# Kernel optimization log

Hardware: AMD Instinct MI355X
Metric: run time of the kernel (lower is better)

## Reference

```python
import jax, jax.numpy as jnp
import numpy as np

HID = 512
VOCAB = 64
SAMPLE_PROB = 0.1


def lstm_cell(x, h, c, w_ih, w_hh, b_ih, b_hh):
    # PyTorch LSTMCell: gates ordered (i, f, g, o)
    gates = x @ w_ih.T + b_ih + h @ w_hh.T + b_hh
    i, f, g, o = jnp.split(gates, 4, axis=-1)
    i = jax.nn.sigmoid(i)
    f = jax.nn.sigmoid(f)
    g = jnp.tanh(g)
    o = jax.nn.sigmoid(o)
    c_new = f * c + i * g
    h_new = o * jnp.tanh(c_new)
    return h_new, c_new


def _linear_params(key, out_dim, in_dim):
    bound = 1.0 / np.sqrt(in_dim)
    kw, kb = jax.random.split(key)
    w = jax.random.uniform(kw, (out_dim, in_dim), jnp.float32, -bound, bound)
    b = jax.random.uniform(kb, (out_dim,), jnp.float32, -bound, bound)
    return w, b


def setup_inputs() -> dict:
    key = jax.random.key(0)
    ks = jax.random.split(key, 9)
    B, R, T = 128, 512, 128
    phi_w, phi_b = _linear_params(ks[0], HID, HID)          # decoder -> context
    psi_w, psi_b = _linear_params(ks[1], HID, HID)          # listener -> context
    w_ih0, b_ih0 = _linear_params(ks[2], 4 * HID, HID + VOCAB)
    w_hh0, b_hh0 = _linear_params(ks[3], 4 * HID, HID)
    w_ih1, b_ih1 = _linear_params(ks[4], 4 * HID, HID)
    w_hh1, b_hh1 = _linear_params(ks[5], 4 * HID, HID)
    out_w, out_b = _linear_params(ks[6], VOCAB, HID)
    h = jax.random.normal(ks[7], (B, R, HID), jnp.float32)
    y = jax.random.randint(ks[8], (B, T + 1), 0, VOCAB)
    return dict(h=h, phi_w=phi_w, phi_b=phi_b, psi_w=psi_w, psi_b=psi_b,
                w_ih0=w_ih0, w_hh0=w_hh0, b_ih0=b_ih0, b_hh0=b_hh0,
                w_ih1=w_ih1, w_hh1=w_hh1, b_ih1=b_ih1, b_hh1=b_hh1,
                out_w=out_w, out_b=out_b, y=y)


def reference(h, phi_w, phi_b, psi_w, psi_b,
              w_ih0, w_hh0, b_ih0, b_hh0,
              w_ih1, w_hh1, b_ih1, b_hh1,
              out_w, out_b, y):
    B = h.shape[0]
    T = y.shape[1] - 1
    # psi is applied to h identically every step; hoist it out of the loop.
    hp = h @ psi_w.T + psi_b                     # [B, R, HID]
    keys = jax.random.split(jax.random.key(42), T)
    z0 = y[:, 0]
    zeros = jnp.zeros((B, HID), h.dtype)
    carry0 = (zeros, zeros, zeros, zeros, z0)    # s0, cs0, s1, cs1, z

    def step(carry, xs):
        s0, cs0, s1, cs1, z = carry
        key, y_next = xs
        z_oh = jax.nn.one_hot(z, VOCAB, dtype=h.dtype)
        # additive-style attention context
        sq = s1 @ phi_w.T + phi_b                # [B, HID]
        e = jnp.einsum('bd,brd->br', sq, hp)     # [B, R]
        alpha = jax.nn.softmax(e, axis=1)
        c = jnp.einsum('br,brd->bd', alpha, hp)  # [B, HID]
        inp = jnp.concatenate([z_oh, c], axis=1)
        s0, cs0 = lstm_cell(inp, s0, cs0, w_ih0, w_hh0, b_ih0, b_hh0)
        s1, cs1 = lstm_cell(s0, s1, cs1, w_ih1, w_hh1, b_ih1, b_hh1)
        o = s1 @ out_w.T + out_b                 # [B, VOCAB]
        k1, k2 = jax.random.split(key)
        sampled = jax.random.categorical(k1, o, axis=1)
        do_sample = jax.random.bernoulli(k2, SAMPLE_PROB, (B,))
        z_next = jnp.where(do_sample, sampled, y_next)
        return (s0, cs0, s1, cs1, z_next), o

    xs = (keys, y[:, 1:].T)                      # per-step key, teacher token [T, B]
    _, outs = jax.lax.scan(step, carry0, xs)     # outs: [T, B, VOCAB]
    return jnp.transpose(outs, (1, 0, 2))        # [B, T, VOCAB]
```

## Files before the change

### kernel.cpp

```cpp
#include <hip/hip_runtime.h>
#include <math.h>


#define JAX_PARTITIONABLE 1

#define B_   128
#define HID_ 512
#define VOC_ 64
#define T_   128

#define S0_OFF    0u
#define CS0_OFF   65536u
#define S1_OFF    131072u
#define CS1_OFF   196608u
#define SQT_OFF   262144u
#define CPR_OFF   327680u
#define AMAT_OFF  393216u
#define W1PSI_OFF 655360u
#define BIAS0_OFF 1703936u
#define V_OFF     1705984u
#define PART_OFF  1706496u
#define GUM_OFF   5900800u
#define UB_OFF    6949376u
#define Z_OFF     6965760u

#define TF_TINY 1.17549435e-38f

__device__ __forceinline__ void tf2x32(unsigned k0, unsigned k1,
                                       unsigned& x0, unsigned& x1) {
  unsigned ks2 = k0 ^ k1 ^ 0x1BD11BDAu;
  const unsigned ks[3] = {k0, k1, ks2};
  const int rot0[4] = {13, 15, 26, 6};
  const int rot1[4] = {17, 29, 16, 24};
  x0 += ks[0]; x1 += ks[1];
  #pragma unroll
  for (int i = 0; i < 5; ++i) {
    #pragma unroll
    for (int r = 0; r < 4; ++r) {
      int rr = (i & 1) ? rot1[r] : rot0[r];
      x0 += x1;
      x1 = (x1 << rr) | (x1 >> (32 - rr));
      x1 ^= x0;
    }
    x0 += ks[(i + 1) % 3];
    x1 += ks[(i + 2) % 3] + (unsigned)(i + 1);
  }
}

__device__ __forceinline__ float bits_to_unit(unsigned bits) {
  return __uint_as_float((bits >> 9) | 0x3f800000u) - 1.0f;
}

__global__ __launch_bounds__(256) void k_random(const int* __restrict__ y,
                                                float* __restrict__ gum,
                                                float* __restrict__ ub,
                                                int* __restrict__ z) {
  int t = blockIdx.x, tid = threadIdx.x;
  unsigned ka, kb, k1a, k1b, k2a, k2b;
#if JAX_PARTITIONABLE
  ka = 0u; kb = (unsigned)t;
  tf2x32(0u, 42u, ka, kb);
  k1a = 0u; k1b = 0u; tf2x32(ka, kb, k1a, k1b);
  k2a = 0u; k2b = 1u; tf2x32(ka, kb, k2a, k2b);
  for (int j = tid; j < B_ * VOC_; j += 256) {
    unsigned x0 = 0u, x1 = (unsigned)j;
    tf2x32(k1a, k1b, x0, x1);
    unsigned bits = x0 ^ x1;
    float f = bits_to_unit(bits);
    float u = fmaxf(TF_TINY, f * (1.0f - TF_TINY) + TF_TINY);
    gum[(size_t)t * (B_ * VOC_) + j] = -logf(-logf(u));
  }
  if (tid < B_) {
    unsigned x0 = 0u, x1 = (unsigned)tid;
    tf2x32(k2a, k2b, x0, x1);
    ub[t * B_ + tid] = bits_to_unit(x0 ^ x1);
  }
#else
  {
    unsigned x0, x1, y0, y1;
    if (t < 64) {
      x0 = 2u * t;     x1 = 128u + 2u * t;     tf2x32(0u, 42u, x0, x1); ka = x0;
      y0 = 2u * t + 1; y1 = 128u + 2u * t + 1; tf2x32(0u, 42u, y0, y1); kb = y0;
    } else {
      x0 = 2u * t - 128u; x1 = 2u * t;         tf2x32(0u, 42u, x0, x1); ka = x1;
      y0 = 2u * t - 127u; y1 = 2u * t + 1;     tf2x32(0u, 42u, y0, y1); kb = y1;
    }
    unsigned e0a = 0u, e0b = 2u; tf2x32(ka, kb, e0a, e0b);
    unsigned e1a = 1u, e1b = 3u; tf2x32(ka, kb, e1a, e1b);
    k1a = e0a; k1b = e1a; k2a = e0b; k2b = e1b;
  }
  for (int j = tid; j < B_ * VOC_; j += 256) {
    unsigned x0, x1, bits;
    if (j < 4096) { x0 = (unsigned)j; x1 = (unsigned)(4096 + j); tf2x32(k1a, k1b, x0, x1); bits = x0; }
    else          { x0 = (unsigned)(j - 4096); x1 = (unsigned)j; tf2x32(k1a, k1b, x0, x1); bits = x1; }
    float f = bits_to_unit(bits);
    float u = fmaxf(TF_TINY, f * (1.0f - TF_TINY) + TF_TINY);
    gum[(size_t)t * (B_ * VOC_) + j] = -logf(-logf(u));
  }
  if (tid < B_) {
    unsigned x0, x1, bits;
    if (tid < 64) { x0 = (unsigned)tid; x1 = (unsigned)(64 + tid); tf2x32(k2a, k2b, x0, x1); bits = x0; }
    else          { x0 = (unsigned)(tid - 64); x1 = (unsigned)tid; tf2x32(k2a, k2b, x0, x1); bits = x1; }
    ub[t * B_ + tid] = bits_to_unit(bits);
  }
#endif
  if (t == 0 && tid < B_) z[tid] = y[tid * (T_ + 1)];
}

__global__ __launch_bounds__(256) void k_fold_misc(
    const float* __restrict__ psi_w, const float* __restrict__ phi_b,
    const float* __restrict__ w_ih0, const float* __restrict__ psi_b,
    const float* __restrict__ b_ih0, const float* __restrict__ b_hh0,
    float* __restrict__ vvec, float* __restrict__ bias0) {
  int gid = blockIdx.x * 256 + threadIdx.x;
  if (gid < 512) {
    float acc = 0.f;
    for (int j = 0; j < 512; ++j) acc += psi_w[j * 512 + gid] * phi_b[j];
    vvec[gid] = acc;
  } else if (gid < 512 + 2048) {
    int j = gid - 512;
    float acc = b_ih0[j] + b_hh0[j];
    const float* wr = w_ih0 + (size_t)j * 576 + 64;
    for (int d = 0; d < 512; ++d) acc += wr[d] * psi_b[d];
    bias0[j] = acc;
  }
}

__global__ __launch_bounds__(256) void k_gemm_tn(
    const float* __restrict__ A, const float* __restrict__ B, float* __restrict__ C,
    int K, int lda, int ldb, int ldc) {
  __shared__ float As[32][33], Bs[32][33];
  int n0 = blockIdx.x * 32, m0 = blockIdx.y * 32;
  int t = threadIdx.x, tx = t & 31, ty = t >> 5;
  float acc[4] = {0.f, 0.f, 0.f, 0.f};
  for (int k0 = 0; k0 < K; k0 += 32) {
    for (int l = t; l < 1024; l += 256) {
      int jj = l >> 5, mm = l & 31;
      As[jj][mm] = A[(size_t)(k0 + jj) * lda + m0 + mm];
      Bs[jj][mm] = B[(size_t)(k0 + jj) * ldb + n0 + mm];
    }
    __syncthreads();
    #pragma unroll 8
    for (int jj = 0; jj < 32; ++jj) {
      float bv = Bs[jj][tx];
      #pragma unroll
      for (int q = 0; q < 4; ++q) acc[q] += As[jj][ty + 8 * q] * bv;
    }
    __syncthreads();
  }
  #pragma unroll
  for (int q = 0; q < 4; ++q) C[(size_t)(m0 + ty + 8 * q) * ldc + n0 + tx] = acc[q];
}

__global__ __launch_bounds__(256) void k_gemm_nn(
    const float* __restrict__ A, const float* __restrict__ B, float* __restrict__ C,
    int K, int lda, int aoff, int ldb, int ldc) {
  __shared__ float As[32][33], Bs[32][33];
  int n0 = blockIdx.x * 32, m0 = blockIdx.y * 32;
  int t = threadIdx.x, tx = t & 31, ty = t >> 5;
  float acc[4] = {0.f, 0.f, 0.f, 0.f};
  for (int k0 = 0; k0 < K; k0 += 32) {
    for (int l = t; l < 1024; l += 256) {
      int r = l >> 5, c = l & 31;
      As[c][r] = A[(size_t)(m0 + r) * lda + aoff + k0 + c];
      Bs[r][c] = B[(size_t)(k0 + r) * ldb + n0 + c];
    }
    __syncthreads();
    #pragma unroll 8
    for (int kk = 0; kk < 32; ++kk) {
      float bv = Bs[kk][tx];
      #pragma unroll
      for (int q = 0; q < 4; ++q) acc[q] += As[kk][ty + 8 * q] * bv;
    }
    __syncthreads();
  }
  #pragma unroll
  for (int q = 0; q < 4; ++q) C[(size_t)(m0 + ty + 8 * q) * ldc + n0 + tx] = acc[q];
}

__global__ __launch_bounds__(256) void k_sqt_init(const float* __restrict__ vvec,
                                                  float* __restrict__ sqt) {
  int lin = blockIdx.x * 256 + threadIdx.x;
  if (lin < B_ * HID_) sqt[lin] = vvec[lin & 511];
}

__global__ __launch_bounds__(256) void k_transpose_ow(const float* __restrict__ outw,
                                                      float* __restrict__ outwT) {
  int gid = blockIdx.x * 256 + threadIdx.x;
  if (gid < 512 * 64) {
    int k = gid >> 6, v = gid & 63;
    outwT[gid] = outw[(size_t)v * 512 + k];
  }
}

__global__ __launch_bounds__(256) void k_attn(const float* __restrict__ h,
                                              const float* __restrict__ sqt,
                                              float* __restrict__ cpr) {
  __shared__ float hs[16 * 512];
  __shared__ float es[16];
  __shared__ float ps[16];
  int b = blockIdx.x, t = threadIdx.x;
  const float* hb = h + (size_t)b * 512 * 512;
  const float* sq = sqt + b * 512;
  int krow = t >> 4, g = t & 15;
  float m = -INFINITY, l = 0.f, a0 = 0.f, a1 = 0.f;
  int d0 = t, d1 = t + 256;
  for (int r0 = 0; r0 < 512; r0 += 16) {
    __syncthreads();
    const float* hr = hb + (size_t)(r0 + krow) * 512;
    float ep = 0.f;
    #pragma unroll
    for (int i = 0; i < 8; ++i) {
      int d = i * 64 + g * 4;
      float4 hv = *(const float4*)(hr + d);
      float4 sv = *(const float4*)(sq + d);
      ep += hv.x * sv.x + hv.y * sv.y + hv.z * sv.z + hv.w * sv.w;
      *(float4*)(&hs[krow * 512 + d]) = hv;
    }
    ep += __shfl_xor(ep, 1);
    ep += __shfl_xor(ep, 2);
    ep += __shfl_xor(ep, 4);
    ep += __shfl_xor(ep, 8);
    if (g == 0) es[krow] = ep;
    __syncthreads();
    float mc = es[0];
    #pragma unroll
    for (int k = 1; k < 16; ++k) mc = fmaxf(mc, es[k]);
    float mn = fmaxf(m, mc);
    if (t < 16) ps[t] = expf(es[t] - mn);
    __syncthreads();
    float sc = expf(m - mn);
    float ls = 0.f;
    float n0 = a0 * sc, n1 = a1 * sc;
    #pragma unroll
    for (int k = 0; k < 16; ++k) {
      float p = ps[k];
      ls += p;
      n0 += p * hs[k * 512 + d0];
      n1 += p * hs[k * 512 + d1];
    }
    m = mn; l = l * sc + ls; a0 = n0; a1 = n1;
  }
  cpr[b * 512 + d0] = a0 / l;
  cpr[b * 512 + d1] = a1 / l;
}

__global__ __launch_bounds__(256) void k_lstm_gemm(
    const float* __restrict__ X0, const float* __restrict__ W0,
    const float* __restrict__ X1, const float* __restrict__ W1,
    float* __restrict__ part) {
  __shared__ float Xs[16][128];
  __shared__ float Ws[16][64];
  int t = threadIdx.x;
  int jt = blockIdx.x * 64;
  int s = blockIdx.y;
  const float* X; const float* W; int kbase;
  if (s < 8) { X = X0; W = W0; kbase = s * 64; }
  else       { X = X1; W = W1; kbase = (s - 8) * 64; }
  float acc[8][4];
  #pragma unroll
  for (int i = 0; i < 8; ++i)
    #pragma unroll
    for (int q = 0; q < 4; ++q) acc[i][q] = 0.f;
  int b0 = (t & 15) * 8, j0 = (t >> 4) * 4;
  for (int kk = 0; kk < 64; kk += 16) {
    #pragma unroll
    for (int lo = 0; lo < 3; ++lo) {
      int u = t + lo * 256;
      if (u < 512) {
        int row = u >> 2;
        int kq = (u & 3) * 4;
        float4 xv = *(const float4*)(X + (size_t)row * 512 + kbase + kk + kq);
        Xs[kq + 0][row] = xv.x; Xs[kq + 1][row] = xv.y;
        Xs[kq + 2][row] = xv.z; Xs[kq + 3][row] = xv.w;
      } else {
        int w = u - 512;
        int row = w >> 2;
        int kq = (w & 3) * 4;
        float4 wv = *(const float4*)(W + (size_t)(jt + row) * 512 + kbase + kk + kq);
        Ws[kq + 0][row] = wv.x; Ws[kq + 1][row] = wv.y;
        Ws[kq + 2][row] = wv.z; Ws[kq + 3][row] = wv.w;
      }
    }
    __syncthreads();
    #pragma unroll
    for (int k = 0; k < 16; ++k) {
      float4 xa = *(const float4*)&Xs[k][b0];
      float4 xb = *(const float4*)&Xs[k][b0 + 4];
      float4 wa = *(const float4*)&Ws[k][j0];
      float xr[8] = {xa.x, xa.y, xa.z, xa.w, xb.x, xb.y, xb.z, xb.w};
      float wr[4] = {wa.x, wa.y, wa.z, wa.w};
      #pragma unroll
      for (int i = 0; i < 8; ++i)
        #pragma unroll
        for (int q = 0; q < 4; ++q) acc[i][q] += xr[i] * wr[q];
    }
    __syncthreads();
  }
  #pragma unroll
  for (int i = 0; i < 8; ++i) {
    float* pr = part + ((size_t)(s * 128 + b0 + i)) * 2048 + jt + j0;
    *(float4*)pr = make_float4(acc[i][0], acc[i][1], acc[i][2], acc[i][3]);
  }
}

__device__ __forceinline__ float sigm(float x) { return 1.0f / (1.0f + expf(-x)); }

__global__ __launch_bounds__(256) void k_lstm_cell(
    const float* __restrict__ part, const float* __restrict__ biasA,
    const float* __restrict__ bi, const float* __restrict__ bh,
    const float* __restrict__ woh, int ldoh,
    const int* __restrict__ z, float* __restrict__ s, float* __restrict__ cs) {
  int lin = blockIdx.x * 256 + threadIdx.x;
  int b = lin >> 9, d = lin & 511;
  int zb = woh ? z[b] : 0;
  float g4[4];
  #pragma unroll
  for (int g = 0; g < 4; ++g) {
    int j = g * 512 + d;
    float sum = biasA ? biasA[j] : (bi[j] + bh[j]);
    if (woh) sum += woh[(size_t)j * ldoh + zb];
    #pragma unroll
    for (int sl = 0; sl < 16; ++sl)
      sum += part[((size_t)(sl * 128 + b)) * 2048 + j];
    g4[g] = sum;
  }
  float ig = sigm(g4[0]), fg = sigm(g4[1]);
  float gg = tanhf(g4[2]), og = sigm(g4[3]);
  float cn = fg * cs[lin] + ig * gg;
  float sn = og * tanhf(cn);
  cs[lin] = cn;
  s[lin] = sn;
}

__global__ __launch_bounds__(512) void k_tail(
    int t, const float* __restrict__ part,
    const float* __restrict__ bi, const float* __restrict__ bh,
    const float* __restrict__ outwT, const float* __restrict__ outb,
    const float* __restrict__ AmatT, const float* __restrict__ vvec,
    const float* __restrict__ gum, const float* __restrict__ ub,
    const int* __restrict__ y, const float* __restrict__ h,
    float* __restrict__ out, float* __restrict__ s1g, float* __restrict__ cs1,
    int* __restrict__ z, float* __restrict__ cpr) {
  __shared__ __align__(16) float hs[64 * 512];
  __shared__ __align__(16) float sl[512];
  __shared__ __align__(16) float sq[512];
  __shared__ float red[256];
  __shared__ float es_l[64];
  int b = blockIdx.x, tid = threadIdx.x;

  {
    int d = tid;
    int lin = b * 512 + d;
    float g4[4];
    #pragma unroll
    for (int g = 0; g < 4; ++g) {
      int j = g * 512 + d;
      float sum = bi[j] + bh[j];
      #pragma unroll
      for (int slc = 0; slc < 16; ++slc)
        sum += part[((size_t)(slc * 128 + b)) * 2048 + j];
      g4[g] = sum;
    }
    float ig = sigm(g4[0]), fg = sigm(g4[1]);
    float gg = tanhf(g4[2]), og = sigm(g4[3]);
    float cn = fg * cs1[lin] + ig * gg;
    float sn = og * tanhf(cn);
    cs1[lin] = cn;
    s1g[lin] = sn;
    sl[d] = sn;
  }
  __syncthreads();

  if (tid < 256) {
    int v = tid & 63, kg = tid >> 6;
    float sum = 0.f;
    #pragma unroll 8
    for (int k = 0; k < 128; k += 4) {
      int kk = kg * 128 + k;
      float q0 = outwT[(size_t)(kk + 0) * 64 + v] * sl[kk + 0];
      float q1 = outwT[(size_t)(kk + 1) * 64 + v] * sl[kk + 1];
      float q2 = outwT[(size_t)(kk + 2) * 64 + v] * sl[kk + 2];
      float q3 = outwT[(size_t)(kk + 3) * 64 + v] * sl[kk + 3];
      sum += q0 + q1 + q2 + q3;
    }
    red[kg * 64 + v] = sum;
  }
  __syncthreads();
  if (tid < 64) {
    float o = red[tid] + red[64 + tid] + red[128 + tid] + red[192 + tid] + outb[tid];
    out[((size_t)b * T_ + t) * VOC_ + tid] = o;
    float val = o + gum[((size_t)t * B_ + b) * VOC_ + tid];
    int idx = tid;
    #pragma unroll
    for (int off = 1; off < 64; off <<= 1) {
      float ov = __shfl_xor(val, off);
      int oi = __shfl_xor(idx, off);
      if (ov > val || (ov == val && oi < idx)) { val = ov; idx = oi; }
    }
    if (tid == 0) {
      float u = ub[t * B_ + b];
      z[b] = (u < 0.1f) ? idx : y[b * (T_ + 1) + t + 1];
    }
  }

  {
    int d = tid;
    float av = vvec[d];
    const float* At = AmatT + d;
    for (int k = 0; k < 512; k += 4) {
      float p0 = At[(size_t)k * 512]       * sl[k];
      float p1 = At[(size_t)(k + 1) * 512] * sl[k + 1];
      float p2 = At[(size_t)(k + 2) * 512] * sl[k + 2];
      float p3 = At[(size_t)(k + 3) * 512] * sl[k + 3];
      av += p0 + p1 + p2 + p3;
    }
    sq[d] = av;
  }
  if (t == T_ - 1) return;
  __syncthreads();

  const float* hb = h + (size_t)b * (512 * 512);
  int krow = tid >> 4;
  int gq = tid & 15;
  int col = gq * 4;
  float4 sqr[8];
  #pragma unroll
  for (int i = 0; i < 8; ++i) sqr[i] = *(const float4*)(&sq[i * 64 + col]);

  float4 hv0[8], hv1[8];
  {
    const float* hr0 = hb + (size_t)krow * 512;
    const float* hr1 = hb + (size_t)(krow + 32) * 512;
    #pragma unroll
    for (int i = 0; i < 8; ++i) {
      hv0[i] = *(const float4*)(hr0 + i * 64 + col);
      hv1[i] = *(const float4*)(hr1 + i * 64 + col);
    }
    float ep0 = 0.f, ep1 = 0.f;
    #pragma unroll
    for (int i = 0; i < 8; ++i) {
      ep0 += hv0[i].x * sqr[i].x + hv0[i].y * sqr[i].y + hv0[i].z * sqr[i].z + hv0[i].w * sqr[i].w;
      *(float4*)(&hs[krow * 512 + i * 64 + col]) = hv0[i];
      ep1 += hv1[i].x * sqr[i].x + hv1[i].y * sqr[i].y + hv1[i].z * sqr[i].z + hv1[i].w * sqr[i].w;
      *(float4*)(&hs[(krow + 32) * 512 + i * 64 + col]) = hv1[i];
    }
    ep0 += __shfl_xor(ep0, 1); ep0 += __shfl_xor(ep0, 2);
    ep0 += __shfl_xor(ep0, 4); ep0 += __shfl_xor(ep0, 8);
    ep1 += __shfl_xor(ep1, 1); ep1 += __shfl_xor(ep1, 2);
    ep1 += __shfl_xor(ep1, 4); ep1 += __shfl_xor(ep1, 8);
    if (gq == 0) { es_l[krow] = ep0; es_l[krow + 32] = ep1; }
  }
  __syncthreads();

  float m = -INFINITY, l = 0.f, a0 = 0.f;
  int d0 = tid;
  int lane15 = tid & 15;
  for (int g = 0; g < 8; ++g) {
    if (g < 7) {
      const float* hr0 = hb + (size_t)((g + 1) * 64 + krow) * 512;
      const float* hr1 = hb + (size_t)((g + 1) * 64 + krow + 32) * 512;
      #pragma unroll
      for (int i = 0; i < 8; ++i) {
        hv0[i] = *(const float4*)(hr0 + i * 64 + col);
        hv1[i] = *(const float4*)(hr1 + i * 64 + col);
      }
    }
    #pragma unroll
    for (int lc = 0; lc < 4; ++lc) {
      float mc = es_l[lc * 16];
      #pragma unroll
      for (int k = 1; k < 16; ++k) mc = fmaxf(mc, es_l[lc * 16 + k]);
      float mn = fmaxf(m, mc);
      float pw = expf(es_l[lc * 16 + lane15] - mn);
      float sc = expf(m - mn);
      float ls = 0.f;
      float n0 = a0 * sc;
      #pragma unroll
      for (int k = 0; k < 16; ++k) {
        float p = __shfl(pw, k);
        ls += p;
        n0 += p * hs[(lc * 16 + k) * 512 + d0];
      }
      m = mn; l = l * sc + ls; a0 = n0;
    }
    __syncthreads();
    if (g < 7) {
      float ep0 = 0.f, ep1 = 0.f;
      #pragma unroll
      for (int i = 0; i < 8; ++i) {
        ep0 += hv0[i].x * sqr[i].x + hv0[i].y * sqr[i].y + hv0[i].z * sqr[i].z + hv0[i].w * sqr[i].w;
        *(float4*)(&hs[krow * 512 + i * 64 + col]) = hv0[i];
        ep1 += hv1[i].x * sqr[i].x + hv1[i].y * sqr[i].y + hv1[i].z * sqr[i].z + hv1[i].w * sqr[i].w;
        *(float4*)(&hs[(krow + 32) * 512 + i * 64 + col]) = hv1[i];
      }
      ep0 += __shfl_xor(ep0, 1); ep0 += __shfl_xor(ep0, 2);
      ep0 += __shfl_xor(ep0, 4); ep0 += __shfl_xor(ep0, 8);
      ep1 += __shfl_xor(ep1, 1); ep1 += __shfl_xor(ep1, 2);
      ep1 += __shfl_xor(ep1, 4); ep1 += __shfl_xor(ep1, 8);
      if (gq == 0) { es_l[krow] = ep0; es_l[krow + 32] = ep1; }
    }
    __syncthreads();
  }
  cpr[b * 512 + d0] = a0 / l;
}

extern "C" void kernel_launch(void* const* d_in, const int* in_sizes, int n_in,
                              void* d_out, int out_size, void* d_ws, size_t ws_size,
                              hipStream_t stream) {
  const float* h     = (const float*)d_in[0];
  const float* phi_w = (const float*)d_in[1];
  const float* phi_b = (const float*)d_in[2];
  const float* psi_w = (const float*)d_in[3];
  const float* psi_b = (const float*)d_in[4];
  const float* w_ih0 = (const float*)d_in[5];
  const float* w_hh0 = (const float*)d_in[6];
  const float* b_ih0 = (const float*)d_in[7];
  const float* b_hh0 = (const float*)d_in[8];
  const float* w_ih1 = (const float*)d_in[9];
  const float* w_hh1 = (const float*)d_in[10];
  const float* b_ih1 = (const float*)d_in[11];
  const float* b_hh1 = (const float*)d_in[12];
  const float* out_w = (const float*)d_in[13];
  const float* out_b = (const float*)d_in[14];
  const int*   y     = (const int*)d_in[15];

  float* out = (float*)d_out;
  float* ws  = (float*)d_ws;

  float* s0    = ws + S0_OFF;
  float* cs0   = ws + CS0_OFF;
  float* s1    = ws + S1_OFF;
  float* cs1   = ws + CS1_OFF;
  float* sqt   = ws + SQT_OFF;
  float* outwT = ws + SQT_OFF;
  float* cpr   = ws + CPR_OFF;
  float* AmatT = ws + AMAT_OFF;
  float* W1psi = ws + W1PSI_OFF;
  float* bias0 = ws + BIAS0_OFF;
  float* vvec  = ws + V_OFF;
  float* part  = ws + PART_OFF;
  float* gum   = ws + GUM_OFF;
  float* ub    = ws + UB_OFF;
  int*   z     = (int*)(ws + Z_OFF);

  hipMemsetAsync(s0, 0, 4 * (size_t)B_ * HID_ * sizeof(float), stream);

  k_random<<<T_, 256, 0, stream>>>(y, gum, ub, z);
  k_fold_misc<<<10, 256, 0, stream>>>(psi_w, phi_b, w_ih0, psi_b, b_ih0, b_hh0, vvec, bias0);
  k_gemm_tn<<<dim3(16, 16), 256, 0, stream>>>(phi_w, psi_w, AmatT, 512, 512, 512, 512);
  k_gemm_nn<<<dim3(16, 64), 256, 0, stream>>>(w_ih0, psi_w, W1psi, 512, 576, 64, 512, 512);
  k_sqt_init<<<256, 256, 0, stream>>>(vvec, sqt);
  k_attn<<<128, 256, 0, stream>>>(h, sqt, cpr);
  k_transpose_ow<<<128, 256, 0, stream>>>(out_w, outwT);

  for (int t = 0; t < T_; ++t) {
    k_lstm_gemm<<<dim3(32, 16), 256, 0, stream>>>(cpr, W1psi, s0, w_hh0, part);
    k_lstm_cell<<<256, 256, 0, stream>>>(part, bias0, nullptr, nullptr, w_ih0, 576, z, s0, cs0);
    k_lstm_gemm<<<dim3(32, 16), 256, 0, stream>>>(s0, w_ih1, s1, w_hh1, part);
    k_tail<<<128, 512, 0, stream>>>(t, part, b_ih1, b_hh1, outwT, out_b, AmatT, vvec,
                                    gum, ub, y, h, out, s1, cs1, z, cpr);
  }
}
```

Measured before the change: 12.55 ms.

## Split per-step attention into two-way split-softmax kernel and fuse RNG into tail

Moves the per-step attention out of the 128-block tail kernel into a separate 256-block kernel in which each block handles half of the 512 encoder rows and writes an unnormalized partial context plus its running max and sum. The next LSTM GEMM merges the two halves using log-sum-exp weights while loading its inputs. The Threefry Gumbel and Bernoulli draws are now computed inline in the tail instead of by a precomputed random kernel, and the z init is folded into the transpose kernel. This doubles the parallelism of the bandwidth-heavy attention pass, at the cost of one extra launch per step and some redundant RNG work per block.

```diff
diff --git a/kernel.cpp b/kernel.cpp
--- a/kernel.cpp
+++ b/kernel.cpp
@@ -1,8 +1,6 @@
 #include <hip/hip_runtime.h>
 #include <math.h>
 
-
-#define JAX_PARTITIONABLE 1
 
 #define B_   128
 #define HID_ 512
@@ -20,8 +18,9 @@
 #define BIAS0_OFF 1703936u
 #define V_OFF     1705984u
 #define PART_OFF  1706496u
-#define GUM_OFF   5900800u
-#define UB_OFF    6949376u
+#define AA_OFF    5900800u
+#define AB_OFF    5966336u
+#define ML_OFF    6031872u
 #define Z_OFF     6965760u
 
 #define TF_TINY 1.17549435e-38f
@@ -49,62 +48,6 @@
 
 __device__ __forceinline__ float bits_to_unit(unsigned bits) {
   return __uint_as_float((bits >> 9) | 0x3f800000u) - 1.0f;
-}
-
-__global__ __launch_bounds__(256) void k_random(const int* __restrict__ y,
-                                                float* __restrict__ gum,
-                                                float* __restrict__ ub,
-                                                int* __restrict__ z) {
-  int t = blockIdx.x, tid = threadIdx.x;
-  unsigned ka, kb, k1a, k1b, k2a, k2b;
-#if JAX_PARTITIONABLE
-  ka = 0u; kb = (unsigned)t;
-  tf2x32(0u, 42u, ka, kb);
-  k1a = 0u; k1b = 0u; tf2x32(ka, kb, k1a, k1b);
-  k2a = 0u; k2b = 1u; tf2x32(ka, kb, k2a, k2b);
-  for (int j = tid; j < B_ * VOC_; j += 256) {
-    unsigned x0 = 0u, x1 = (unsigned)j;
-    tf2x32(k1a, k1b, x0, x1);
-    unsigned bits = x0 ^ x1;
-    float f = bits_to_unit(bits);
-    float u = fmaxf(TF_TINY, f * (1.0f - TF_TINY) + TF_TINY);
-    gum[(size_t)t * (B_ * VOC_) + j] = -logf(-logf(u));
-  }
-  if (tid < B_) {
-    unsigned x0 = 0u, x1 = (unsigned)tid;
-    tf2x32(k2a, k2b, x0, x1);
-    ub[t * B_ + tid] = bits_to_unit(x0 ^ x1);
-  }
-#else
-  {
-    unsigned x0, x1, y0, y1;
-    if (t < 64) {
-      x0 = 2u * t;     x1 = 128u + 2u * t;     tf2x32(0u, 42u, x0, x1); ka = x0;
-      y0 = 2u * t + 1; y1 = 128u + 2u * t + 1; tf2x32(0u, 42u, y0, y1); kb = y0;
-    } else {
-      x0 = 2u * t - 128u; x1 = 2u * t;         tf2x32(0u, 42u, x0, x1); ka = x1;
-      y0 = 2u * t - 127u; y1 = 2u * t + 1;     tf2x32(0u, 42u, y0, y1); kb = y1;
-    }
-    unsigned e0a = 0u, e0b = 2u; tf2x32(ka, kb, e0a, e0b);
-    unsigned e1a = 1u, e1b = 3u; tf2x32(ka, kb, e1a, e1b);
-    k1a = e0a; k1b = e1a; k2a = e0b; k2b = e1b;
-  }
-  for (int j = tid; j < B_ * VOC_; j += 256) {
-    unsigned x0, x1, bits;
-    if (j < 4096) { x0 = (unsigned)j; x1 = (unsigned)(4096 + j); tf2x32(k1a, k1b, x0, x1); bits = x0; }
-    else          { x0 = (unsigned)(j - 4096); x1 = (unsigned)j; tf2x32(k1a, k1b, x0, x1); bits = x1; }
-    float f = bits_to_unit(bits);
-    float u = fmaxf(TF_TINY, f * (1.0f - TF_TINY) + TF_TINY);
-    gum[(size_t)t * (B_ * VOC_) + j] = -logf(-logf(u));
-  }
-  if (tid < B_) {
-    unsigned x0, x1, bits;
-    if (tid < 64) { x0 = (unsigned)tid; x1 = (unsigned)(64 + tid); tf2x32(k2a, k2b, x0, x1); bits = x0; }
-    else          { x0 = (unsigned)(tid - 64); x1 = (unsigned)tid; tf2x32(k2a, k2b, x0, x1); bits = x1; }
-    ub[t * B_ + tid] = bits_to_unit(bits);
-  }
-#endif
-  if (t == 0 && tid < B_) z[tid] = y[tid * (T_ + 1)];
 }
 
 __global__ __launch_bounds__(256) void k_fold_misc(
@@ -184,65 +127,193 @@
   if (lin < B_ * HID_) sqt[lin] = vvec[lin & 511];
 }
 
-__global__ __launch_bounds__(256) void k_transpose_ow(const float* __restrict__ outw,
-                                                      float* __restrict__ outwT) {
+__global__ __launch_bounds__(256) void k_transpose_owz(
+    const float* __restrict__ outw, float* __restrict__ outwT,
+    const int* __restrict__ y, int* __restrict__ z) {
   int gid = blockIdx.x * 256 + threadIdx.x;
   if (gid < 512 * 64) {
     int k = gid >> 6, v = gid & 63;
     outwT[gid] = outw[(size_t)v * 512 + k];
   }
-}
-
-__global__ __launch_bounds__(256) void k_attn(const float* __restrict__ h,
-                                              const float* __restrict__ sqt,
-                                              float* __restrict__ cpr) {
-  __shared__ float hs[16 * 512];
-  __shared__ float es[16];
-  __shared__ float ps[16];
-  int b = blockIdx.x, t = threadIdx.x;
-  const float* hb = h + (size_t)b * 512 * 512;
-  const float* sq = sqt + b * 512;
-  int krow = t >> 4, g = t & 15;
-  float m = -INFINITY, l = 0.f, a0 = 0.f, a1 = 0.f;
-  int d0 = t, d1 = t + 256;
-  for (int r0 = 0; r0 < 512; r0 += 16) {
-    __syncthreads();
-    const float* hr = hb + (size_t)(r0 + krow) * 512;
-    float ep = 0.f;
+  if (gid < B_) z[gid] = y[gid * (T_ + 1)];
+}
+
+__global__ __launch_bounds__(512) void k_attn2(
+    const float* __restrict__ h, const float* __restrict__ sqt,
+    float* __restrict__ aA, float* __restrict__ aB, float* __restrict__ ml) {
+  __shared__ __align__(16) float hs[64 * 512];
+  __shared__ float es_l[64];
+  int bid = blockIdx.x, tid = threadIdx.x;
+  int b = bid & 127, half = bid >> 7;
+  int R0 = half * 256;
+  const float* hb = h + (size_t)b * (512 * 512);
+  const float* sqg = sqt + b * 512;
+  int krow = tid >> 4;
+  int gq = tid & 15;
+  int col = gq * 4;
+  float4 sqr[8];
+  #pragma unroll
+  for (int i = 0; i < 8; ++i) sqr[i] = *(const float4*)(sqg + i * 64 + col);
+
+  float4 hv0[8], hv1[8];
+  {
+    const float* hr0 = hb + (size_t)(R0 + krow) * 512;
+    const float* hr1 = hb + (size_t)(R0 + krow + 32) * 512;
     #pragma unroll
     for (int i = 0; i < 8; ++i) {
-      int d = i * 64 + g * 4;
-      float4 hv = *(const float4*)(hr + d);
-      float4 sv = *(const float4*)(sq + d);
-      ep += hv.x * sv.x + hv.y * sv.y + hv.z * sv.z + hv.w * sv.w;
-      *(float4*)(&hs[krow * 512 + d]) = hv;
-    }
-    ep += __shfl_xor(ep, 1);
-    ep += __shfl_xor(ep, 2);
-    ep += __shfl_xor(ep, 4);
-    ep += __shfl_xor(ep, 8);
-    if (g == 0) es[krow] = ep;
-    __syncthreads();
-    float mc = es[0];
-    #pragma unroll
-    for (int k = 1; k < 16; ++k) mc = fmaxf(mc, es[k]);
-    float mn = fmaxf(m, mc);
-    if (t < 16) ps[t] = expf(es[t] - mn);
-    __syncthreads();
-    float sc = expf(m - mn);
-    float ls = 0.f;
-    float n0 = a0 * sc, n1 = a1 * sc;
+      hv0[i] = *(const float4*)(hr0 + i * 64 + col);
+      hv1[i] = *(const float4*)(hr1 + i * 64 + col);
+    }
+    float ep0 = 0.f, ep1 = 0.f;
+    #pragma unroll
+    for (int i = 0; i < 8; ++i) {
+      ep0 += hv0[i].x * sqr[i].x + hv0[i].y * sqr[i].y + hv0[i].z * sqr[i].z + hv0[i].w * sqr[i].w;
+      *(float4*)(&hs[krow * 512 + i * 64 + col]) = hv0[i];
+      ep1 += hv1[i].x * sqr[i].x + hv1[i].y * sqr[i].y + hv1[i].z * sqr[i].z + hv1[i].w * sqr[i].w;
+      *(float4*)(&hs[(krow + 32) * 512 + i * 64 + col]) = hv1[i];
+    }
+    ep0 += __shfl_xor(ep0, 1); ep0 += __shfl_xor(ep0, 2);
+    ep0 += __shfl_xor(ep0, 4); ep0 += __shfl_xor(ep0, 8);
+    ep1 += __shfl_xor(ep1, 1); ep1 += __shfl_xor(ep1, 2);
+    ep1 += __shfl_xor(ep1, 4); ep1 += __shfl_xor(ep1, 8);
+    if (gq == 0) { es_l[krow] = ep0; es_l[krow + 32] = ep1; }
+  }
+  __syncthreads();
+
+  float m = -INFINITY, l = 0.f, a0 = 0.f;
+  int d0 = tid;
+  int lane15 = tid & 15;
+  for (int g = 0; g < 4; ++g) {
+    if (g < 3) {
+      const float* hr0 = hb + (size_t)(R0 + (g + 1) * 64 + krow) * 512;
+      const float* hr1 = hb + (size_t)(R0 + (g + 1) * 64 + krow + 32) * 512;
+      #pragma unroll
+      for (int i = 0; i < 8; ++i) {
+        hv0[i] = *(const float4*)(hr0 + i * 64 + col);
+        hv1[i] = *(const float4*)(hr1 + i * 64 + col);
+      }
+    }
+    #pragma unroll
+    for (int lc = 0; lc < 4; ++lc) {
+      float mc = es_l[lc * 16];
+      #pragma unroll
+      for (int k = 1; k < 16; ++k) mc = fmaxf(mc, es_l[lc * 16 + k]);
+      float mn = fmaxf(m, mc);
+      float pw = expf(es_l[lc * 16 + lane15] - mn);
+      float sc = expf(m - mn);
+      float ls = 0.f;
+      float n0 = a0 * sc;
+      #pragma unroll
+      for (int k = 0; k < 16; ++k) {
+        float p = __shfl(pw, k);
+        ls += p;
+        n0 += p * hs[(lc * 16 + k) * 512 + d0];
+      }
+      m = mn; l = l * sc + ls; a0 = n0;
+    }
+    __syncthreads();
+    if (g < 3) {
+      float ep0 = 0.f, ep1 = 0.f;
+      #pragma unroll
+      for (int i = 0; i < 8; ++i) {
+        ep0 += hv0[i].x * sqr[i].x + hv0[i].y * sqr[i].y + hv0[i].z * sqr[i].z + hv0[i].w * sqr[i].w;
+        *(float4*)(&hs[krow * 512 + i * 64 + col]) = hv0[i];
+        ep1 += hv1[i].x * sqr[i].x + hv1[i].y * sqr[i].y + hv1[i].z * sqr[i].z + hv1[i].w * sqr[i].w;
+        *(float4*)(&hs[(krow + 32) * 512 + i * 64 + col]) = hv1[i];
+      }
+      ep0 += __shfl_xor(ep0, 1); ep0 += __shfl_xor(ep0, 2);
+      ep0 += __shfl_xor(ep0, 4); ep0 += __shfl_xor(ep0, 8);
+      ep1 += __shfl_xor(ep1, 1); ep1 += __shfl_xor(ep1, 2);
+      ep1 += __shfl_xor(ep1, 4); ep1 += __shfl_xor(ep1, 8);
+      if (gq == 0) { es_l[krow] = ep0; es_l[krow + 32] = ep1; }
+    }
+    __syncthreads();
+  }
+  float* aH = half ? aB : aA;
+  aH[(size_t)b * 512 + d0] = a0;
+  if (tid == 0) {
+    ml[half * 256 + b] = m;
+    ml[half * 256 + 128 + b] = l;
+  }
+}
+
+__global__ __launch_bounds__(256) void k_gemm0m(
+    const float* __restrict__ aA, const float* __restrict__ aB,
+    const float* __restrict__ ml,
+    const float* __restrict__ W0, const float* __restrict__ X1,
+    const float* __restrict__ W1, float* __restrict__ part) {
+  __shared__ float Xs[16][128];
+  __shared__ float Ws[16][64];
+  __shared__ float cA[128], cB[128];
+  int t = threadIdx.x;
+  int jt = blockIdx.x * 64;
+  int s = blockIdx.y;
+  int kbase = (s & 7) * 64;
+  if (s < 8 && t < 128) {
+    float mA = ml[t], lA = ml[128 + t];
+    float mB = ml[256 + t], lB = ml[384 + t];
+    float mm = fmaxf(mA, mB);
+    float eA = expf(mA - mm), eB = expf(mB - mm);
+    float L = lA * eA + lB * eB;
+    cA[t] = eA / L;
+    cB[t] = eB / L;
+  }
+  __syncthreads();
+  float acc[8][4];
+  #pragma unroll
+  for (int i = 0; i < 8; ++i)
+    #pragma unroll
+    for (int q = 0; q < 4; ++q) acc[i][q] = 0.f;
+  int b0 = (t & 15) * 8, j0 = (t >> 4) * 4;
+  const float* W = (s < 8) ? W0 : W1;
+  for (int kk = 0; kk < 64; kk += 16) {
+    #pragma unroll
+    for (int lo = 0; lo < 3; ++lo) {
+      int u = t + lo * 256;
+      if (u < 512) {
+        int row = u >> 2;
+        int kq = (u & 3) * 4;
+        float4 xv;
+        if (s < 8) {
+          float4 a4 = *(const float4*)(aA + (size_t)row * 512 + kbase + kk + kq);
+          float4 b4 = *(const float4*)(aB + (size_t)row * 512 + kbase + kk + kq);
+          float ca = cA[row], cb = cB[row];
+          xv = make_float4(a4.x * ca + b4.x * cb, a4.y * ca + b4.y * cb,
+                           a4.z * ca + b4.z * cb, a4.w * ca + b4.w * cb);
+        } else {
+          xv = *(const float4*)(X1 + (size_t)row * 512 + kbase + kk + kq);
+        }
+        Xs[kq + 0][row] = xv.x; Xs[kq + 1][row] = xv.y;
+        Xs[kq + 2][row] = xv.z; Xs[kq + 3][row] = xv.w;
+      } else {
+        int w = u - 512;
+        int row = w >> 2;
+        int kq = (w & 3) * 4;
+        float4 wv = *(const float4*)(W + (size_t)(jt + row) * 512 + kbase + kk + kq);
+        Ws[kq + 0][row] = wv.x; Ws[kq + 1][row] = wv.y;
+        Ws[kq + 2][row] = wv.z; Ws[kq + 3][row] = wv.w;
+      }
+    }
+    __syncthreads();
     #pragma unroll
     for (int k = 0; k < 16; ++k) {
-      float p = ps[k];
-      ls += p;
-      n0 += p * hs[k * 512 + d0];
-      n1 += p * hs[k * 512 + d1];
-    }
-    m = mn; l = l * sc + ls; a0 = n0; a1 = n1;
-  }
-  cpr[b * 512 + d0] = a0 / l;
-  cpr[b * 512 + d1] = a1 / l;
+      float4 xa = *(const float4*)&Xs[k][b0];
+      float4 xb = *(const float4*)&Xs[k][b0 + 4];
+      float4 wa = *(const float4*)&Ws[k][j0];
+      float xr[8] = {xa.x, xa.y, xa.z, xa.w, xb.x, xb.y, xb.z, xb.w};
+      float wr[4] = {wa.x, wa.y, wa.z, wa.w};
+      #pragma unroll
+      for (int i = 0; i < 8; ++i)
+        #pragma unroll
+        for (int q = 0; q < 4; ++q) acc[i][q] += xr[i] * wr[q];
+    }
+    __syncthreads();
+  }
+  #pragma unroll
+  for (int i = 0; i < 8; ++i) {
+    float* pr = part + ((size_t)(s * 128 + b0 + i)) * 2048 + jt + j0;
+    *(float4*)pr = make_float4(acc[i][0], acc[i][1], acc[i][2], acc[i][3]);
+  }
 }
 
 __global__ __launch_bounds__(256) void k_lstm_gemm(
@@ -333,20 +404,16 @@
   s[lin] = sn;
 }
 
-__global__ __launch_bounds__(512) void k_tail(
+__global__ __launch_bounds__(512) void k_mid(
     int t, const float* __restrict__ part,
     const float* __restrict__ bi, const float* __restrict__ bh,
     const float* __restrict__ outwT, const float* __restrict__ outb,
     const float* __restrict__ AmatT, const float* __restrict__ vvec,
-    const float* __restrict__ gum, const float* __restrict__ ub,
-    const int* __restrict__ y, const float* __restrict__ h,
+    const int* __restrict__ y,
     float* __restrict__ out, float* __restrict__ s1g, float* __restrict__ cs1,
-    int* __restrict__ z, float* __restrict__ cpr) {
-  __shared__ __align__(16) float hs[64 * 512];
+    int* __restrict__ z, float* __restrict__ sqt) {
   __shared__ __align__(16) float sl[512];
-  __shared__ __align__(16) float sq[512];
   __shared__ float red[256];
-  __shared__ float es_l[64];
   int b = blockIdx.x, tid = threadIdx.x;
 
   {
@@ -390,7 +457,17 @@
   if (tid < 64) {
     float o = red[tid] + red[64 + tid] + red[128 + tid] + red[192 + tid] + outb[tid];
     out[((size_t)b * T_ + t) * VOC_ + tid] = o;
-    float val = o + gum[((size_t)t * B_ + b) * VOC_ + tid];
+    unsigned ka = 0u, kb = (unsigned)t;
+    tf2x32(0u, 42u, ka, kb);
+    unsigned k1a = 0u, k1b = 0u;
+    tf2x32(ka, kb, k1a, k1b);
+    unsigned x0 = 0u, x1 = (unsigned)(b * VOC_ + tid);
+    tf2x32(k1a, k1b, x0, x1);
+    unsigned bits = x0 ^ x1;
+    float f = bits_to_unit(bits);
+    float u = fmaxf(TF_TINY, f * (1.0f - TF_TINY) + TF_TINY);
+    float gumv = -logf(-logf(u));
+    float val = o + gumv;
     int idx = tid;
     #pragma unroll
     for (int off = 1; off < 64; off <<= 1) {
@@ -399,8 +476,12 @@
       if (ov > val || (ov == val && oi < idx)) { val = ov; idx = oi; }
     }
     if (tid == 0) {
-      float u = ub[t * B_ + b];
-      z[b] = (u < 0.1f) ? idx : y[b * (T_ + 1) + t + 1];
+      unsigned k2a = 0u, k2b = 1u;
+      tf2x32(ka, kb, k2a, k2b);
+      unsigned u0 = 0u, u1 = (unsigned)b;
+      tf2x32(k2a, k2b, u0, u1);
+      float ub = bits_to_unit(u0 ^ u1);
+      z[b] = (ub < 0.1f) ? idx : y[b * (T_ + 1) + t + 1];
     }
   }
 
@@ -415,94 +496,8 @@
       float p3 = At[(size_t)(k + 3) * 512] * sl[k + 3];
       av += p0 + p1 + p2 + p3;
     }
-    sq[d] = av;
-  }
-  if (t == T_ - 1) return;
-  __syncthreads();
-
-  const float* hb = h + (size_t)b * (512 * 512);
-  int krow = tid >> 4;
-  int gq = tid & 15;
-  int col = gq * 4;
-  float4 sqr[8];
-  #pragma unroll
-  for (int i = 0; i < 8; ++i) sqr[i] = *(const float4*)(&sq[i * 64 + col]);
-
-  float4 hv0[8], hv1[8];
-  {
-    const float* hr0 = hb + (size_t)krow * 512;
-    const float* hr1 = hb + (size_t)(krow + 32) * 512;
-    #pragma unroll
-    for (int i = 0; i < 8; ++i) {
-      hv0[i] = *(const float4*)(hr0 + i * 64 + col);
-      hv1[i] = *(const float4*)(hr1 + i * 64 + col);
-    }
-    float ep0 = 0.f, ep1 = 0.f;
-    #pragma unroll
-    for (int i = 0; i < 8; ++i) {
-      ep0 += hv0[i].x * sqr[i].x + hv0[i].y * sqr[i].y + hv0[i].z * sqr[i].z + hv0[i].w * sqr[i].w;
-      *(float4*)(&hs[krow * 512 + i * 64 + col]) = hv0[i];
-      ep1 += hv1[i].x * sqr[i].x + hv1[i].y * sqr[i].y + hv1[i].z * sqr[i].z + hv1[i].w * sqr[i].w;
-      *(float4*)(&hs[(krow + 32) * 512 + i * 64 + col]) = hv1[i];
-    }
-    ep0 += __shfl_xor(ep0, 1); ep0 += __shfl_xor(ep0, 2);
-    ep0 += __shfl_xor(ep0, 4); ep0 += __shfl_xor(ep0, 8);
-    ep1 += __shfl_xor(ep1, 1); ep1 += __shfl_xor(ep1, 2);
-    ep1 += __shfl_xor(ep1, 4); ep1 += __shfl_xor(ep1, 8);
-    if (gq == 0) { es_l[krow] = ep0; es_l[krow + 32] = ep1; }
-  }
-  __syncthreads();
-
-  float m = -INFINITY, l = 0.f, a0 = 0.f;
-  int d0 = tid;
-  int lane15 = tid & 15;
-  for (int g = 0; g < 8; ++g) {
-    if (g < 7) {
-      const float* hr0 = hb + (size_t)((g + 1) * 64 + krow) * 512;
-      const float* hr1 = hb + (size_t)((g + 1) * 64 + krow + 32) * 512;
-      #pragma unroll
-      for (int i = 0; i < 8; ++i) {
-        hv0[i] = *(const float4*)(hr0 + i * 64 + col);
-        hv1[i] = *(const float4*)(hr1 + i * 64 + col);
-      }
-    }
-    #pragma unroll
-    for (int lc = 0; lc < 4; ++lc) {
-      float mc = es_l[lc * 16];
-      #pragma unroll
-      for (int k = 1; k < 16; ++k) mc = fmaxf(mc, es_l[lc * 16 + k]);
-      float mn = fmaxf(m, mc);
-      float pw = expf(es_l[lc * 16 + lane15] - mn);
-      float sc = expf(m - mn);
-      float ls = 0.f;
-      float n0 = a0 * sc;
-      #pragma unroll
-      for (int k = 0; k < 16; ++k) {
-        float p = __shfl(pw, k);
-        ls += p;
-        n0 += p * hs[(lc * 16 + k) * 512 + d0];
-      }
-      m = mn; l = l * sc + ls; a0 = n0;
-    }
-    __syncthreads();
-    if (g < 7) {
-      float ep0 = 0.f, ep1 = 0.f;
-      #pragma unroll
-      for (int i = 0; i < 8; ++i) {
-        ep0 += hv0[i].x * sqr[i].x + hv0[i].y * sqr[i].y + hv0[i].z * sqr[i].z + hv0[i].w * sqr[i].w;
-        *(float4*)(&hs[krow * 512 + i * 64 + col]) = hv0[i];
-        ep1 += hv1[i].x * sqr[i].x + hv1[i].y * sqr[i].y + hv1[i].z * sqr[i].z + hv1[i].w * sqr[i].w;
-        *(float4*)(&hs[(krow + 32) * 512 + i * 64 + col]) = hv1[i];
-      }
-      ep0 += __shfl_xor(ep0, 1); ep0 += __shfl_xor(ep0, 2);
-      ep0 += __shfl_xor(ep0, 4); ep0 += __shfl_xor(ep0, 8);
-      ep1 += __shfl_xor(ep1, 1); ep1 += __shfl_xor(ep1, 2);
-      ep1 += __shfl_xor(ep1, 4); ep1 += __shfl_xor(ep1, 8);
-      if (gq == 0) { es_l[krow] = ep0; es_l[krow + 32] = ep1; }
-    }
-    __syncthreads();
-  }
-  cpr[b * 512 + d0] = a0 / l;
+    sqt[b * 512 + d] = av;
+  }
 }
 
 extern "C" void kernel_launch(void* const* d_in, const int* in_sizes, int n_in,
@@ -533,32 +528,34 @@
   float* s1    = ws + S1_OFF;
   float* cs1   = ws + CS1_OFF;
   float* sqt   = ws + SQT_OFF;
-  float* outwT = ws + SQT_OFF;
-  float* cpr   = ws + CPR_OFF;
+  float* outwT = ws + CPR_OFF;
   float* AmatT = ws + AMAT_OFF;
   float* W1psi = ws + W1PSI_OFF;
   float* bias0 = ws + BIAS0_OFF;
   float* vvec  = ws + V_OFF;
   float* part  = ws + PART_OFF;
-  float* gum   = ws + GUM_OFF;
-  float* ub    = ws + UB_OFF;
+  float* aA    = ws + AA_OFF;
+  float* aB    = ws + AB_OFF;
+  float* ml    = ws + ML_OFF;
   int*   z     = (int*)(ws + Z_OFF);
 
   hipMemsetAsync(s0, 0, 4 * (size_t)B_ * HID_ * sizeof(float), stream);
 
-  k_random<<<T_, 256, 0, stream>>>(y, gum, ub, z);
   k_fold_misc<<<10, 256, 0, stream>>>(psi_w, phi_b, w_ih0, psi_b, b_ih0, b_hh0, vvec, bias0);
   k_gemm_tn<<<dim3(16, 16), 256, 0, stream>>>(phi_w, psi_w, AmatT, 512, 512, 512, 512);
   k_gemm_nn<<<dim3(16, 64), 256, 0, stream>>>(w_ih0, psi_w, W1psi, 512, 576, 64, 512, 512);
+  k_transpose_owz<<<128, 256, 0, stream>>>(out_w, outwT, y, z);
   k_sqt_init<<<256, 256, 0, stream>>>(vvec, sqt);
-  k_attn<<<128, 256, 0, stream>>>(h, sqt, cpr);
-  k_transpose_ow<<<128, 256, 0, stream>>>(out_w, outwT);
+  k_attn2<<<256, 512, 0, stream>>>(h, sqt, aA, aB, ml);
 
   for (int t = 0; t < T_; ++t) {
-    k_lstm_gemm<<<dim3(32, 16), 256, 0, stream>>>(cpr, W1psi, s0, w_hh0, part);
+    k_gemm0m<<<dim3(32, 16), 256, 0, stream>>>(aA, aB, ml, W1psi, s0, w_hh0, part);
     k_lstm_cell<<<256, 256, 0, stream>>>(part, bias0, nullptr, nullptr, w_ih0, 576, z, s0, cs0);
     k_lstm_gemm<<<dim3(32, 16), 256, 0, stream>>>(s0, w_ih1, s1, w_hh1, part);
-    k_tail<<<128, 512, 0, stream>>>(t, part, b_ih1, b_hh1, outwT, out_b, AmatT, vvec,
-                                    gum, ub, y, h, out, s1, cs1, z, cpr);
-  }
-}
+    k_mid<<<128, 512, 0, stream>>>(t, part, b_ih1, b_hh1, outwT, out_b, AmatT, vvec,
+                                   y, out, s1, cs1, z, sqt);
+    if (t < T_ - 1) {
+      k_attn2<<<256, 512, 0, stream>>>(h, sqt, aA, aB, ml);
+    }
+  }
+}
```

Result: faster. 11.32 ms (-9.8%).
